# Optimization experiments

Measured on AMD Instinct MI355X. Metric: run time of the kernel, lower is better.

## Reference

```python
import jax, jax.numpy as jnp
import numpy as np


def setup_inputs() -> dict:
    key = jax.random.key(0)
    ks = jax.random.split(key, 7)
    B, T, K, H, A = 32, 32, 196, 512, 512
    # Xavier-normal-ish scale for square 512x512 linears
    s = float(np.sqrt(2.0 / (H + A)))
    return {
        "att_feats": jax.random.normal(ks[0], (B, K, H), jnp.float32),
        "hiddens": jax.random.normal(ks[1], (B, T, H), jnp.float32),
        "sentinel": jax.random.normal(ks[2], (B, T, H), jnp.float32),
        "Wv": jax.random.normal(ks[3], (H, A), jnp.float32) * s,
        "Wg": jax.random.normal(ks[4], (H, A), jnp.float32) * s,
        "Ws": jax.random.normal(ks[5], (H, A), jnp.float32) * s,
        "wh": jax.random.normal(ks[6], (A,), jnp.float32) * s,
    }


def reference(att_feats, hiddens, sentinel, Wv, Wg, Ws, wh):
    # Dropout treated as identity (eval mode / deterministic reference).
    cv = jnp.einsum("bkh,ha->bka", att_feats, Wv)          # [B,K,A]
    cg = jnp.einsum("bth,ha->bta", hiddens, Wg)            # [B,T,A]
    # Broadcast additive attention: [B,T,K,A]
    content_v = cv[:, None, :, :] + cg[:, :, None, :]
    z_t = jnp.einsum("btka,a->btk", jnp.tanh(content_v), wh)  # [B,T,K]
    alpha_t = jax.nn.softmax(z_t, axis=-1)                    # [B,T,K]
    c_t = jnp.einsum("btk,bkh->bth", alpha_t, att_feats)      # [B,T,H]
    # Sentinel branch
    content_s = jnp.einsum("bth,ha->bta", sentinel, Ws) + cg  # [B,T,A]
    z_ext = jnp.einsum("bta,a->bt", jnp.tanh(content_s), wh)[..., None]  # [B,T,1]
    extended = jnp.concatenate([z_t, z_ext], axis=2)          # [B,T,K+1]
    alpha_hat = jax.nn.softmax(extended, axis=-1)
    beta_t = alpha_hat[:, :, -1:]                             # [B,T,1]
    c_hat_t = beta_t * sentinel + (1.0 - beta_t) * c_t        # [B,T,H]
    return (c_hat_t, alpha_t, beta_t)
```

## Files before the change

### kernel.cpp

```cpp
#include <hip/hip_runtime.h>
#include <hip/hip_bf16.h>
#include <math.h>

#define HDIM 512
#define ADIM 512
#define BATCH 32
#define TDIM 32
#define KDIM 196
#define MROWS 8320
#define ZSC 2.885390081777927f
#define ZT_N 200704

typedef short short8 __attribute__((ext_vector_type(8)));
typedef float floatx4 __attribute__((ext_vector_type(4)));

__device__ __forceinline__ void gl_lds16(const __hip_bfloat16* g, __hip_bfloat16* l) {
    __builtin_amdgcn_global_load_lds(
        (const __attribute__((address_space(1))) unsigned int*)(const void*)g,
        (__attribute__((address_space(3))) unsigned int*)(void*)l, 16, 0, 0);
}

__device__ __forceinline__ float tanh_ps(float up) {
    float e = __builtin_amdgcn_exp2f(up);
    float r = __builtin_amdgcn_rcpf(e + 1.0f);
    return fmaf(-2.0f, r, 1.0f);
}

__global__ __launch_bounds__(256) void convB(const float* __restrict__ Wv,
                                             const float* __restrict__ Wg,
                                             const float* __restrict__ Ws,
                                             __hip_bfloat16* __restrict__ bthi,
                                             __hip_bfloat16* __restrict__ btlo) {
    __shared__ float tile[64][65];
    const int tid = threadIdx.x;
    const int bid = blockIdx.x;
    const int mz  = bid >> 6;
    const int rem = bid & 63;
    const int k0  = (rem >> 3) * 64;
    const int n0  = (rem & 7) * 64;
    const float* src = mz == 0 ? Wv : (mz == 1 ? Wg : Ws);
    #pragma unroll
    for (int i = 0; i < 16; ++i) {
        int k = (tid >> 6) * 16 + i;
        int n = tid & 63;
        tile[k][n] = src[(size_t)(k0 + k) * 512 + n0 + n];
    }
    __syncthreads();
    const size_t obase = (size_t)mz * 262144;
    #pragma unroll
    for (int i = 0; i < 16; ++i) {
        int n = (tid >> 6) * 16 + i;
        int k = tid & 63;
        float x = tile[k][n];
        __hip_bfloat16 h = __float2bfloat16(x);
        __hip_bfloat16 l = __float2bfloat16(x - __bfloat162float(h));
        size_t o = obase + (size_t)(n0 + n) * 512 + k0 + k;
        bthi[o] = h;
        btlo[o] = l;
    }
}

__global__ __launch_bounds__(256) void gemm_bf16x3(
        const float* __restrict__ att, const float* __restrict__ hid,
        const float* __restrict__ sen,
        const __hip_bfloat16* __restrict__ Bthi, const __hip_bfloat16* __restrict__ Btlo,
        float* __restrict__ C) {
    __shared__ __hip_bfloat16 smem[12288];

    const int tid  = threadIdx.x;
    const int lane = tid & 63;
    const int wave = tid >> 6;
    const int wm = wave >> 1;
    const int wn = wave & 1;
    const int row0 = blockIdx.x * 64;
    const int col0 = blockIdx.y * 128;
    const int seg = (row0 < 6272) ? 0 : ((row0 < 7296) ? 1 : 2);
    const float* Asrc = seg == 0 ? att : (seg == 1 ? hid : sen);
    const int arow0 = row0 - (seg == 0 ? 0 : (seg == 1 ? 6272 : 7296));
    const __hip_bfloat16* Bh = Bthi + (size_t)seg * 262144;
    const __hip_bfloat16* Bl = Btlo + (size_t)seg * 262144;

    floatx4 acc[2][4];
    #pragma unroll
    for (int i = 0; i < 2; ++i)
        #pragma unroll
        for (int j = 0; j < 4; ++j)
            acc[i][j] = (floatx4){0.f, 0.f, 0.f, 0.f};

    const int kq8 = (lane >> 4) << 3;
    const int a_row = tid >> 2;
    const int a_k   = (tid & 3) << 3;

    for (int k0 = 0; k0 < 512; k0 += 32) {
        #pragma unroll
        for (int s = 0; s < 4; ++s) {
            int u = tid + (s << 8);
            if (u < 512) {
                gl_lds16(Bh + (size_t)(col0 + (u >> 2)) * 512 + k0 + ((u & 3) << 3),
                         smem + 4096 + u * 8);
            } else {
                int v = u - 512;
                gl_lds16(Bl + (size_t)(col0 + (v >> 2)) * 512 + k0 + ((v & 3) << 3),
                         smem + 8192 + v * 8);
            }
        }
        {
            const float* ap = Asrc + (size_t)(arow0 + a_row) * 512 + k0 + a_k;
            float4 v0 = *(const float4*)ap;
            float4 v1 = *(const float4*)(ap + 4);
            float x[8] = {v0.x, v0.y, v0.z, v0.w, v1.x, v1.y, v1.z, v1.w};
            union { __hip_bfloat16 h[8]; short8 v; } Hi, Lo;
            #pragma unroll
            for (int i = 0; i < 8; ++i) {
                Hi.h[i] = __float2bfloat16(x[i]);
                Lo.h[i] = __float2bfloat16(x[i] - __bfloat162float(Hi.h[i]));
            }
            *(short8*)(smem + a_row * 32 + a_k)        = Hi.v;
            *(short8*)(smem + 2048 + a_row * 32 + a_k) = Lo.v;
        }
        asm volatile("s_waitcnt vmcnt(0)" ::: "memory");
        __syncthreads();

        short8 a_hi[2], a_lo[2], b_hi[4], b_lo[4];
        #pragma unroll
        for (int i = 0; i < 2; ++i) {
            int m = wm * 32 + i * 16 + (lane & 15);
            a_hi[i] = *(const short8*)(smem + m * 32 + kq8);
            a_lo[i] = *(const short8*)(smem + 2048 + m * 32 + kq8);
        }
        #pragma unroll
        for (int j = 0; j < 4; ++j) {
            int n = wn * 64 + j * 16 + (lane & 15);
            b_hi[j] = *(const short8*)(smem + 4096 + n * 32 + kq8);
            b_lo[j] = *(const short8*)(smem + 8192 + n * 32 + kq8);
        }

        #pragma unroll
        for (int i = 0; i < 2; ++i)
            #pragma unroll
            for (int j = 0; j < 4; ++j) {
                acc[i][j] = __builtin_amdgcn_mfma_f32_16x16x32_bf16(a_hi[i], b_hi[j], acc[i][j], 0, 0, 0);
                acc[i][j] = __builtin_amdgcn_mfma_f32_16x16x32_bf16(a_hi[i], b_lo[j], acc[i][j], 0, 0, 0);
                acc[i][j] = __builtin_amdgcn_mfma_f32_16x16x32_bf16(a_lo[i], b_hi[j], acc[i][j], 0, 0, 0);
            }
        __syncthreads();
    }

    #pragma unroll
    for (int i = 0; i < 2; ++i) {
        #pragma unroll
        for (int r = 0; r < 4; ++r) {
            int row = row0 + wm * 32 + i * 16 + ((lane >> 4) << 2) + r;
            float* cp = C + (size_t)row * 512 + col0 + wn * 64 + (lane & 15);
            #pragma unroll
            for (int j = 0; j < 4; ++j) cp[j * 16] = acc[i][j][r] * ZSC;
        }
    }
}

__global__ __launch_bounds__(256) void z_kernel(const float* __restrict__ cv,
                                                const float* __restrict__ cg,
                                                const float* __restrict__ wh,
                                                float* __restrict__ z_part) {
    __shared__ float cvs[8][132];
    __shared__ float cgs[32][132];
    __shared__ float whs[132];

    const int kb  = blockIdx.x;
    const int b   = blockIdx.y;
    const int ha  = blockIdx.z;
    const int tid = threadIdx.x;
    const int t       = tid & 31;
    const int k_local = tid >> 5;
    const int k       = kb * 8 + k_local;
    const bool do_z = (k < KDIM);

    const int r_st = tid >> 5;
    const int q_st = tid & 31;

    float acc = 0.f, acc2 = 0.f;

    for (int c = 0; c < 2; ++c) {
        const int a0 = (ha * 2 + c) * 128;
        __syncthreads();
        {
            int kr = kb * 8 + r_st;
            if (kr < KDIM)
                *(float4*)&cvs[r_st][4 * q_st] =
                    *(const float4*)(cv + ((size_t)b * KDIM + kr) * ADIM + a0 + 4 * q_st);
        }
        #pragma unroll
        for (int s = 0; s < 4; ++s) {
            int idx = tid + s * 256;
            int rr = idx >> 5, qq = idx & 31;
            *(float4*)&cgs[rr][4 * qq] =
                *(const float4*)(cg + ((size_t)b * TDIM + rr) * ADIM + a0 + 4 * qq);
        }
        if (tid < 32)
            *(float4*)&whs[4 * tid] = *(const float4*)(wh + a0 + 4 * tid);
        __syncthreads();

        if (do_z) {
            #pragma unroll 8
            for (int q = 0; q < 32; ++q) {
                float4 v  = *(const float4*)&cvs[k_local][4 * q];
                float4 g  = *(const float4*)&cgs[t][4 * q];
                float4 w4 = *(const float4*)&whs[4 * q];
                acc  = fmaf(w4.x, tanh_ps(v.x + g.x), acc);
                acc2 = fmaf(w4.y, tanh_ps(v.y + g.y), acc2);
                acc  = fmaf(w4.z, tanh_ps(v.z + g.z), acc);
                acc2 = fmaf(w4.w, tanh_ps(v.w + g.w), acc2);
            }
        }
    }

    if (do_z)
        z_part[(size_t)ha * ZT_N + ((size_t)b * TDIM + t) * KDIM + k] = acc + acc2;
}

__global__ __launch_bounds__(256) void out_kernel(const float* __restrict__ z_part,
                                                  const float* __restrict__ cs,
                                                  const float* __restrict__ cg,
                                                  const float* __restrict__ wh,
                                                  const float* __restrict__ att,
                                                  const float* __restrict__ sen,
                                                  float* __restrict__ out_chat,
                                                  float* __restrict__ out_alpha,
                                                  float* __restrict__ out_beta) {
    __shared__ float alpha_s[4][200];
    __shared__ float beta_s[4];

    const int tg = blockIdx.x;
    const int b  = blockIdx.y;
    const int hs = blockIdx.z;
    const int tid  = threadIdx.x;
    const int wave = tid >> 6;
    const int lane = tid & 63;
    const int t = tg * 4 + wave;
    const int h = hs * 256 + tid;

    const float* csrow = cs + ((size_t)b * TDIM + t) * ADIM;
    const float* cgrow = cg + ((size_t)b * TDIM + t) * ADIM;
    float p = 0.f;
    #pragma unroll
    for (int hh = 0; hh < 2; ++hh) {
        float4 sv = *(const float4*)(csrow + 8 * lane + 4 * hh);
        float4 gv = *(const float4*)(cgrow + 8 * lane + 4 * hh);
        float4 w4 = *(const float4*)(wh + 8 * lane + 4 * hh);
        p = fmaf(w4.x, tanh_ps(sv.x + gv.x), p);
        p = fmaf(w4.y, tanh_ps(sv.y + gv.y), p);
        p = fmaf(w4.z, tanh_ps(sv.z + gv.z), p);
        p = fmaf(w4.w, tanh_ps(sv.w + gv.w), p);
    }
    #pragma unroll
    for (int off = 32; off; off >>= 1) p += __shfl_xor(p, off, 64);
    const float se = p;

    const float* zrow0 = z_part + ((size_t)b * TDIM + t) * KDIM;
    const float* zrow1 = zrow0 + ZT_N;
    float z0 = zrow0[lane]       + zrow1[lane];
    float z1 = zrow0[lane + 64]  + zrow1[lane + 64];
    float z2 = zrow0[lane + 128] + zrow1[lane + 128];
    float z3 = (lane < 4) ? (zrow0[lane + 192] + zrow1[lane + 192]) : -INFINITY;

    float m = fmaxf(fmaxf(z0, z1), fmaxf(z2, z3));
    #pragma unroll
    for (int off = 32; off; off >>= 1) m = fmaxf(m, __shfl_xor(m, off, 64));

    float e0 = __expf(z0 - m), e1 = __expf(z1 - m);
    float e2 = __expf(z2 - m), e3 = (lane < 4) ? __expf(z3 - m) : 0.0f;
    float s = e0 + e1 + e2 + e3;
    #pragma unroll
    for (int off = 32; off; off >>= 1) s += __shfl_xor(s, off, 64);

    float invS = 1.0f / s;
    float a0 = e0 * invS, a1 = e1 * invS, a2 = e2 * invS, a3 = e3 * invS;

    alpha_s[wave][lane] = a0;
    alpha_s[wave][lane + 64] = a1;
    alpha_s[wave][lane + 128] = a2;
    if (lane < 4) alpha_s[wave][lane + 192] = a3;
    if (hs == 0) {
        float* arow = out_alpha + ((size_t)b * TDIM + t) * KDIM;
        arow[lane] = a0;
        arow[lane + 64] = a1;
        arow[lane + 128] = a2;
        if (lane < 4) arow[lane + 192] = a3;
    }

    float m2 = fmaxf(m, se);
    float eext = __expf(se - m2);
    float S2 = s * __expf(m - m2) + eext;
    float beta = eext / S2;
    if (lane == 0) {
        beta_s[wave] = beta;
        if (hs == 0) out_beta[b * TDIM + t] = beta;
    }
    __syncthreads();

    const float* attb = att + (size_t)b * KDIM * HDIM;
    float acc[4] = {};
    #pragma unroll 8
    for (int k = 0; k < KDIM; ++k) {
        float av = attb[(size_t)k * HDIM + h];
        #pragma unroll
        for (int w = 0; w < 4; ++w)
            acc[w] = fmaf(alpha_s[w][k], av, acc[w]);
    }

    #pragma unroll
    for (int w = 0; w < 4; ++w) {
        int tt = tg * 4 + w;
        float bt = beta_s[w];
        float om = 1.0f - bt;
        size_t o = ((size_t)b * TDIM + tt) * HDIM;
        out_chat[o + h] = fmaf(bt, sen[o + h], om * acc[w]);
    }
}

__global__ __launch_bounds__(256) void gemm_f32(const float* __restrict__ Amat,
                                                const float* __restrict__ Bmat,
                                                float* __restrict__ Cmat) {
    __shared__ float As[16][64 + 4];
    __shared__ float Bs[16][64];
    const int tid = threadIdx.x;
    const int tx = tid & 15;
    const int ty = tid >> 4;
    const int row0 = blockIdx.x * 64;
    const int col0 = blockIdx.y * 64;
    float acc[4][4] = {};
    for (int k0 = 0; k0 < HDIM; k0 += 16) {
        #pragma unroll
        for (int i = 0; i < 4; ++i) {
            int idx = tid + i * 256;
            As[idx & 15][idx >> 4] = Amat[(size_t)(row0 + (idx >> 4)) * HDIM + k0 + (idx & 15)];
        }
        #pragma unroll
        for (int i = 0; i < 4; ++i) {
            int idx = tid + i * 256;
            Bs[idx >> 6][idx & 63] = Bmat[(size_t)(k0 + (idx >> 6)) * ADIM + col0 + (idx & 63)];
        }
        __syncthreads();
        #pragma unroll
        for (int k = 0; k < 16; ++k) {
            float4 a4 = *(const float4*)&As[k][ty * 4];
            float4 b4 = *(const float4*)&Bs[k][tx * 4];
            float a[4] = {a4.x, a4.y, a4.z, a4.w};
            float b[4] = {b4.x, b4.y, b4.z, b4.w};
            #pragma unroll
            for (int i = 0; i < 4; ++i)
                #pragma unroll
                for (int j = 0; j < 4; ++j)
                    acc[i][j] += a[i] * b[j];
        }
        __syncthreads();
    }
    #pragma unroll
    for (int i = 0; i < 4; ++i) {
        size_t r = (size_t)(row0 + ty * 4 + i) * ADIM + col0 + tx * 4;
        #pragma unroll
        for (int j = 0; j < 4; ++j) Cmat[r + j] = acc[i][j] * ZSC;
    }
}

__global__ __launch_bounds__(256) void zero_fill(float* __restrict__ p, int n) {
    int i = blockIdx.x * 256 + threadIdx.x;
    if (i < n) p[i] = 0.f;
}

extern "C" void kernel_launch(void* const* d_in, const int* in_sizes, int n_in,
                              void* d_out, int out_size, void* d_ws, size_t ws_size,
                              hipStream_t stream) {
    const float* att = (const float*)d_in[0];
    const float* hid = (const float*)d_in[1];
    const float* sen = (const float*)d_in[2];
    const float* Wv  = (const float*)d_in[3];
    const float* Wg  = (const float*)d_in[4];
    const float* Ws  = (const float*)d_in[5];
    const float* wh  = (const float*)d_in[6];

    float* out = (float*)d_out;
    float* out_chat  = out;
    float* out_alpha = out + 524288;
    float* out_beta  = out + 524288 + 200704;

    char* wsb = (char*)d_ws;
    const size_t C_BYTES  = (size_t)MROWS * 512 * 4;
    const size_t ZT_BYTES = (size_t)2 * ZT_N * 4;
    const size_t BT_BYTES = (size_t)3 * 512 * 512 * 2;
    const size_t need = C_BYTES + ZT_BYTES + 2 * BT_BYTES;

    float* C  = (float*)wsb;
    float* cv = C;
    float* cg = C + 6272 * 512;
    float* cs = C + 7296 * 512;
    float* zt = (float*)(wsb + C_BYTES);

    if (ws_size >= need) {
        __hip_bfloat16* bthi = (__hip_bfloat16*)(wsb + C_BYTES + ZT_BYTES);
        __hip_bfloat16* btlo = bthi + (size_t)3 * 512 * 512;

        convB<<<192, 256, 0, stream>>>(Wv, Wg, Ws, bthi, btlo);
        gemm_bf16x3<<<dim3(130, 4), 256, 0, stream>>>(att, hid, sen, bthi, btlo, C);
    } else {
        gemm_f32<<<dim3(98, 8), 256, 0, stream>>>(att, Wv, cv);
        gemm_f32<<<dim3(16, 8), 256, 0, stream>>>(hid, Wg, cg);
        gemm_f32<<<dim3(16, 8), 256, 0, stream>>>(sen, Ws, cs);
    }

    z_kernel<<<dim3(25, 32, 2), 256, 0, stream>>>(cv, cg, wh, zt);

    out_kernel<<<dim3(8, 32, 2), 256, 0, stream>>>(zt, cs, cg, wh, att, sen,
                                                   out_chat, out_alpha, out_beta);
}
```

Baseline: 146.3 us.

## Pair tanh reciprocals in z kernel and shrink GEMM column tile to 64

The z kernel rewrites tanh(x) as 1 - 2/(exp2(x)+1) and combines two terms over a common denominator, so each pair of tanh-weighted terms needs one reciprocal instead of two. The weight sum is accumulated separately and folded in at the end. The goal is fewer transcendental ops in the dominant z computation, at some risk of overflow when the product of two denominators becomes large. The split-bf16 GEMM also halves its column tile to 64 and doubles the grid, trading more A reloads for more blocks and less LDS per block.

```diff
diff --git a/kernel.cpp b/kernel.cpp
--- a/kernel.cpp
+++ b/kernel.cpp
@@ -60,12 +60,16 @@
     }
 }
 
+#define GA_HI 0
+#define GA_LO 2048
+#define GB_HI 4096
+#define GB_LO 6144
 __global__ __launch_bounds__(256) void gemm_bf16x3(
         const float* __restrict__ att, const float* __restrict__ hid,
         const float* __restrict__ sen,
         const __hip_bfloat16* __restrict__ Bthi, const __hip_bfloat16* __restrict__ Btlo,
         float* __restrict__ C) {
-    __shared__ __hip_bfloat16 smem[12288];
+    __shared__ __hip_bfloat16 smem[8192];
 
     const int tid  = threadIdx.x;
     const int lane = tid & 63;
@@ -73,37 +77,29 @@
     const int wm = wave >> 1;
     const int wn = wave & 1;
     const int row0 = blockIdx.x * 64;
-    const int col0 = blockIdx.y * 128;
+    const int col0 = blockIdx.y * 64;
     const int seg = (row0 < 6272) ? 0 : ((row0 < 7296) ? 1 : 2);
     const float* Asrc = seg == 0 ? att : (seg == 1 ? hid : sen);
     const int arow0 = row0 - (seg == 0 ? 0 : (seg == 1 ? 6272 : 7296));
     const __hip_bfloat16* Bh = Bthi + (size_t)seg * 262144;
     const __hip_bfloat16* Bl = Btlo + (size_t)seg * 262144;
 
-    floatx4 acc[2][4];
+    floatx4 acc[2][2];
     #pragma unroll
     for (int i = 0; i < 2; ++i)
         #pragma unroll
-        for (int j = 0; j < 4; ++j)
+        for (int j = 0; j < 2; ++j)
             acc[i][j] = (floatx4){0.f, 0.f, 0.f, 0.f};
 
-    const int kq8 = (lane >> 4) << 3;
+    const int kq8   = (lane >> 4) << 3;
     const int a_row = tid >> 2;
     const int a_k   = (tid & 3) << 3;
+    const int b_n   = tid >> 2;
+    const int b_k   = (tid & 3) << 3;
 
     for (int k0 = 0; k0 < 512; k0 += 32) {
-        #pragma unroll
-        for (int s = 0; s < 4; ++s) {
-            int u = tid + (s << 8);
-            if (u < 512) {
-                gl_lds16(Bh + (size_t)(col0 + (u >> 2)) * 512 + k0 + ((u & 3) << 3),
-                         smem + 4096 + u * 8);
-            } else {
-                int v = u - 512;
-                gl_lds16(Bl + (size_t)(col0 + (v >> 2)) * 512 + k0 + ((v & 3) << 3),
-                         smem + 8192 + v * 8);
-            }
-        }
+        gl_lds16(Bh + (size_t)(col0 + b_n) * 512 + k0 + b_k, smem + GB_HI + b_n * 32 + b_k);
+        gl_lds16(Bl + (size_t)(col0 + b_n) * 512 + k0 + b_k, smem + GB_LO + b_n * 32 + b_k);
         {
             const float* ap = Asrc + (size_t)(arow0 + a_row) * 512 + k0 + a_k;
             float4 v0 = *(const float4*)ap;
@@ -115,30 +111,30 @@
                 Hi.h[i] = __float2bfloat16(x[i]);
                 Lo.h[i] = __float2bfloat16(x[i] - __bfloat162float(Hi.h[i]));
             }
-            *(short8*)(smem + a_row * 32 + a_k)        = Hi.v;
-            *(short8*)(smem + 2048 + a_row * 32 + a_k) = Lo.v;
+            *(short8*)(smem + GA_HI + a_row * 32 + a_k) = Hi.v;
+            *(short8*)(smem + GA_LO + a_row * 32 + a_k) = Lo.v;
         }
         asm volatile("s_waitcnt vmcnt(0)" ::: "memory");
         __syncthreads();
 
-        short8 a_hi[2], a_lo[2], b_hi[4], b_lo[4];
+        short8 a_hi[2], a_lo[2], b_hi[2], b_lo[2];
         #pragma unroll
         for (int i = 0; i < 2; ++i) {
             int m = wm * 32 + i * 16 + (lane & 15);
-            a_hi[i] = *(const short8*)(smem + m * 32 + kq8);
-            a_lo[i] = *(const short8*)(smem + 2048 + m * 32 + kq8);
-        }
-        #pragma unroll
-        for (int j = 0; j < 4; ++j) {
-            int n = wn * 64 + j * 16 + (lane & 15);
-            b_hi[j] = *(const short8*)(smem + 4096 + n * 32 + kq8);
-            b_lo[j] = *(const short8*)(smem + 8192 + n * 32 + kq8);
+            a_hi[i] = *(const short8*)(smem + GA_HI + m * 32 + kq8);
+            a_lo[i] = *(const short8*)(smem + GA_LO + m * 32 + kq8);
+        }
+        #pragma unroll
+        for (int j = 0; j < 2; ++j) {
+            int n = wn * 32 + j * 16 + (lane & 15);
+            b_hi[j] = *(const short8*)(smem + GB_HI + n * 32 + kq8);
+            b_lo[j] = *(const short8*)(smem + GB_LO + n * 32 + kq8);
         }
 
         #pragma unroll
         for (int i = 0; i < 2; ++i)
             #pragma unroll
-            for (int j = 0; j < 4; ++j) {
+            for (int j = 0; j < 2; ++j) {
                 acc[i][j] = __builtin_amdgcn_mfma_f32_16x16x32_bf16(a_hi[i], b_hi[j], acc[i][j], 0, 0, 0);
                 acc[i][j] = __builtin_amdgcn_mfma_f32_16x16x32_bf16(a_hi[i], b_lo[j], acc[i][j], 0, 0, 0);
                 acc[i][j] = __builtin_amdgcn_mfma_f32_16x16x32_bf16(a_lo[i], b_hi[j], acc[i][j], 0, 0, 0);
@@ -151,9 +147,9 @@
         #pragma unroll
         for (int r = 0; r < 4; ++r) {
             int row = row0 + wm * 32 + i * 16 + ((lane >> 4) << 2) + r;
-            float* cp = C + (size_t)row * 512 + col0 + wn * 64 + (lane & 15);
+            float* cp = C + (size_t)row * 512 + col0 + wn * 32 + (lane & 15);
             #pragma unroll
-            for (int j = 0; j < 4; ++j) cp[j * 16] = acc[i][j][r] * ZSC;
+            for (int j = 0; j < 2; ++j) cp[j * 16] = acc[i][j][r] * ZSC;
         }
     }
 }
@@ -178,26 +174,26 @@
     const int r_st = tid >> 5;
     const int q_st = tid & 31;
 
-    float acc = 0.f, acc2 = 0.f;
+    float acc = 0.f, acc2 = 0.f, wsum = 0.f;
 
     for (int c = 0; c < 2; ++c) {
-        const int a0 = (ha * 2 + c) * 128;
+        const int a0c = (ha * 2 + c) * 128;
         __syncthreads();
         {
             int kr = kb * 8 + r_st;
             if (kr < KDIM)
                 *(float4*)&cvs[r_st][4 * q_st] =
-                    *(const float4*)(cv + ((size_t)b * KDIM + kr) * ADIM + a0 + 4 * q_st);
+                    *(const float4*)(cv + ((size_t)b * KDIM + kr) * ADIM + a0c + 4 * q_st);
         }
         #pragma unroll
         for (int s = 0; s < 4; ++s) {
             int idx = tid + s * 256;
             int rr = idx >> 5, qq = idx & 31;
             *(float4*)&cgs[rr][4 * qq] =
-                *(const float4*)(cg + ((size_t)b * TDIM + rr) * ADIM + a0 + 4 * qq);
+                *(const float4*)(cg + ((size_t)b * TDIM + rr) * ADIM + a0c + 4 * qq);
         }
         if (tid < 32)
-            *(float4*)&whs[4 * tid] = *(const float4*)(wh + a0 + 4 * tid);
+            *(float4*)&whs[4 * tid] = *(const float4*)(wh + a0c + 4 * tid);
         __syncthreads();
 
         if (do_z) {
@@ -206,16 +202,26 @@
                 float4 v  = *(const float4*)&cvs[k_local][4 * q];
                 float4 g  = *(const float4*)&cgs[t][4 * q];
                 float4 w4 = *(const float4*)&whs[4 * q];
-                acc  = fmaf(w4.x, tanh_ps(v.x + g.x), acc);
-                acc2 = fmaf(w4.y, tanh_ps(v.y + g.y), acc2);
-                acc  = fmaf(w4.z, tanh_ps(v.z + g.z), acc);
-                acc2 = fmaf(w4.w, tanh_ps(v.w + g.w), acc2);
+                float E0 = __builtin_amdgcn_exp2f(v.x + g.x);
+                float E1 = __builtin_amdgcn_exp2f(v.y + g.y);
+                float E2 = __builtin_amdgcn_exp2f(v.z + g.z);
+                float E3 = __builtin_amdgcn_exp2f(v.w + g.w);
+                float a0 = E0 + 1.0f, a1 = E1 + 1.0f;
+                float a2 = E2 + 1.0f, a3 = E3 + 1.0f;
+                float n01 = fmaf(w4.x, a1, w4.y * a0);
+                float n23 = fmaf(w4.z, a3, w4.w * a2);
+                float r01 = __builtin_amdgcn_rcpf(a0 * a1);
+                float r23 = __builtin_amdgcn_rcpf(a2 * a3);
+                acc  = fmaf(n01, r01, acc);
+                acc2 = fmaf(n23, r23, acc2);
+                wsum += (w4.x + w4.y) + (w4.z + w4.w);
             }
         }
     }
 
     if (do_z)
-        z_part[(size_t)ha * ZT_N + ((size_t)b * TDIM + t) * KDIM + k] = acc + acc2;
+        z_part[(size_t)ha * ZT_N + ((size_t)b * TDIM + t) * KDIM + k] =
+            fmaf(-2.0f, acc + acc2, wsum);
 }
 
 __global__ __launch_bounds__(256) void out_kernel(const float* __restrict__ z_part,
@@ -363,11 +369,6 @@
     }
 }
 
-__global__ __launch_bounds__(256) void zero_fill(float* __restrict__ p, int n) {
-    int i = blockIdx.x * 256 + threadIdx.x;
-    if (i < n) p[i] = 0.f;
-}
-
 extern "C" void kernel_launch(void* const* d_in, const int* in_sizes, int n_in,
                               void* d_out, int out_size, void* d_ws, size_t ws_size,
                               hipStream_t stream) {
@@ -401,7 +402,7 @@
         __hip_bfloat16* btlo = bthi + (size_t)3 * 512 * 512;
 
         convB<<<192, 256, 0, stream>>>(Wv, Wg, Ws, bthi, btlo);
-        gemm_bf16x3<<<dim3(130, 4), 256, 0, stream>>>(att, hid, sen, bthi, btlo, C);
+        gemm_bf16x3<<<dim3(130, 8), 256, 0, stream>>>(att, hid, sen, bthi, btlo, C);
     } else {
         gemm_f32<<<dim3(98, 8), 256, 0, stream>>>(att, Wv, cv);
         gemm_f32<<<dim3(16, 8), 256, 0, stream>>>(hid, Wg, cg);
```

Result: slower. 149.8 us (+2.4%).
